# Performance work log

Measured on AMD Instinct MI355X. Metric: run time of the kernel, lower is better.

## Reference

```python
import jax, jax.numpy as jnp
import numpy as np

B, S, D, H, L = 128, 256, 128, 4, 2
N = S - 1            # tree nodes (complete binary tree, depths 0..7)
MAX_DEPTH = 7
NEG = -1e9
EPS = 1e-6


def _binary_tree_topology():
    n = np.arange(N)
    parent = np.where(n > 0, (n - 1) // 2, 0).astype(np.int32)   # parent(0) dummy
    depth = np.floor(np.log2(n + 1)).astype(np.int32)            # BFS level
    is_leaf = (2 * n + 1 >= N)
    return parent, depth, is_leaf


def setup_inputs() -> dict:
    key = jax.random.key(0)
    ks = jax.random.split(key, 6)
    p_np, d_np, l_np = _binary_tree_topology()
    parent = jnp.broadcast_to(jnp.asarray(p_np), (B, N))
    depth = jnp.broadcast_to(jnp.asarray(d_np), (B, N))
    is_leaf = jnp.broadcast_to(jnp.asarray(l_np), (B, N))
    x = jax.random.normal(ks[0], (B, S, D), jnp.float32)
    mask = jnp.zeros((B, 1, 1, S), jnp.float32)  # full trees -> no padding
    sc = 1.0 / np.sqrt(D)
    Wq = jax.random.normal(ks[1], (L, D, D), jnp.float32) * sc
    Wk = jax.random.normal(ks[2], (L, D, D), jnp.float32) * sc
    Wv = jax.random.normal(ks[3], (L, D, D), jnp.float32) * sc
    Wo = jax.random.normal(ks[4], (L, D, D), jnp.float32) * sc
    bq = jnp.zeros((L, D)); bk = jnp.zeros((L, D)); bv = jnp.zeros((L, D)); bo = jnp.zeros((L, D))
    g1 = jnp.ones((L, D)); b1 = jnp.zeros((L, D))
    g2 = jnp.ones((L, D)); b2 = jnp.zeros((L, D))
    return dict(x=x, mask=mask, parent=parent, depth=depth, is_leaf=is_leaf,
                Wq=Wq, bq=bq, Wk=Wk, bk=bk, Wv=Wv, bv=bv, Wo=Wo, bo=bo,
                g1=g1, b1=b1, g2=g2, b2=b2)


def _layernorm(x, g, b):
    mu = jnp.mean(x, axis=-1, keepdims=True)
    var = jnp.mean(jnp.square(x - mu), axis=-1, keepdims=True)
    return g * (x - mu) * jax.lax.rsqrt(var + EPS) + b


def _tree_agg(x, parent, depth, is_leaf):
    """Vectorized bottom-up tree aggregation (agg='sum': tanh(sum children)).
    Seq positions map to tree nodes in BFS order; last position passes through."""
    e = x[:, :N]                                            # [B, N, D]
    seg = (parent + (jnp.arange(B) * N)[:, None]).reshape(-1)  # flat parent ids
    for d in range(MAX_DEPTH, 0, -1):                       # deepest level -> root
        contrib = jnp.where((depth == d)[..., None], e, 0.0)
        agg = jax.ops.segment_sum(contrib.reshape(B * N, D), seg,
                                  num_segments=B * N).reshape(B, N, D)
        upd = ((depth == d - 1) & (~is_leaf))[..., None]    # internal nodes at d-1
        e = jnp.where(upd, jnp.tanh(agg), e)
    return jnp.concatenate([e, x[:, N:]], axis=1)


def reference(x, mask, parent, depth, is_leaf,
              Wq, bq, Wk, bk, Wv, bv, Wo, bo, g1, b1, g2, b2):
    Dh = D // H
    scale = 1.0 / jnp.sqrt(jnp.float32(Dh))
    losses = []
    weights = None
    for l in range(L):
        q = (jnp.einsum('bsd,de->bse', x, Wq[l]) + bq[l]).reshape(B, S, H, Dh).transpose(0, 2, 1, 3)
        k = (jnp.einsum('bsd,de->bse', x, Wk[l]) + bk[l]).reshape(B, S, H, Dh).transpose(0, 2, 1, 3)
        v = (jnp.einsum('bsd,de->bse', x, Wv[l]) + bv[l]).reshape(B, S, H, Dh).transpose(0, 2, 1, 3)
        logits = jnp.einsum('bhqd,bhkd->bhqk', q, k) * scale + mask * NEG
        attn = jax.nn.softmax(logits, axis=-1)              # [B, H, S, S]
        ctx = jnp.einsum('bhqk,bhkd->bhqd', attn, v).transpose(0, 2, 1, 3).reshape(B, S, D)
        att_out = jnp.einsum('bsd,de->bse', ctx, Wo[l]) + bo[l]
        out1 = _layernorm(x + att_out, g1[l], b1[l])
        tab = _tree_agg(out1, parent, depth, is_leaf)       # dropout: eval -> identity
        x = _layernorm(out1 + tab, g2[l], b2[l])
        weights = attn[:, :, -1, :]
        losses.append(jnp.sum(jnp.abs(weights)))
    total_l1 = jnp.sum(jnp.stack(losses))
    return x, total_l1, weights
```

## Files before the change

kernel.cpp:

```cpp
#include <hip/hip_runtime.h>
#include <math.h>

typedef __bf16 bf16x8 __attribute__((ext_vector_type(8)));
typedef __bf16 bf16x4 __attribute__((ext_vector_type(4)));
typedef __bf16 bf16x2 __attribute__((ext_vector_type(2)));
typedef float f32x4 __attribute__((ext_vector_type(4)));

namespace {
constexpr int kB = 128, kS = 256, kD = 128, kH = 4;
constexpr float kEps = 1e-6f;
constexpr float kScale = 0.17677669529663687f;
constexpr float kNeg = -1000000000.0f;
constexpr float kLog2e = 1.4426950408889634f;
constexpr size_t kSZ = (size_t)kB * kS * kD;
}

__device__ __forceinline__ void glds16(const void* g, void* l) {
    __builtin_amdgcn_global_load_lds(
        (const __attribute__((address_space(1))) unsigned int*)g,
        (__attribute__((address_space(3))) unsigned int*)l, 16, 0, 0);
}

__global__ __launch_bounds__(256) void wtrans(
    const float* __restrict__ Wq, const float* __restrict__ Wk,
    const float* __restrict__ Wv, const float* __restrict__ Wo,
    __bf16* __restrict__ Wt)
{
    const int mtx = blockIdx.x & 3, l = blockIdx.x >> 2;
    const float* W = (mtx == 0 ? Wq : mtx == 1 ? Wk : mtx == 2 ? Wv : Wo) +
                     (size_t)l * kD * kD;
    __bf16* o = Wt + (size_t)blockIdx.x * kD * kD;
    for (int idx = threadIdx.x; idx < kD * kD; idx += 256) {
        const int k = idx >> 7, n = idx & 127;
        const int lo = n & 15, ni = n >> 4;
        const int j = k & 7, tt = k >> 3, g = tt & 3, ks = tt >> 2;
        o[((ni * 4 + ks) * 64 + g * 16 + lo) * 8 + j] = (__bf16)W[idx];
    }
}

template <int WEIGHTS, bool F32X>
__global__ __launch_bounds__(512) void mega_attn(
    const void* __restrict__ xsrc, const __bf16* __restrict__ Wp,
    const float* __restrict__ bq, const float* __restrict__ bk,
    const float* __restrict__ bv, const float* __restrict__ bo,
    const float* __restrict__ mask, const float* __restrict__ gamma,
    const float* __restrict__ beta, __bf16* __restrict__ O1,
    float* __restrict__ wout, float* __restrict__ l1out)
{
    __shared__ __bf16 Xs[256 * 128];
    __shared__ __bf16 Kls[256 * 32];
    __shared__ __bf16 Vt[32][276];
    __shared__ __bf16 Pl[8][16 * 64];
    __shared__ __bf16 Qs[8][16 * 32];
    __shared__ __bf16 Ctx[128 * 128];
    __shared__ float mb[256];

    const int t = threadIdx.x;
    const int w = t >> 6, l = t & 63, lo = l & 15, g = l >> 4;
    const int b = blockIdx.x & 127, strip = blockIdx.x >> 7;
    const int q0 = strip * 128 + w * 16;
    const int tk0 = w * 32;
    const int kswz = (lo ^ (lo >> 2)) & 3;

    const __bf16* Wqp = Wp;
    const __bf16* Wkp = Wp + 16384;
    const __bf16* Wvp = Wp + 2 * 16384;
    const __bf16* Wop = Wp + 3 * 16384;

    if constexpr (F32X) {
#pragma unroll
        for (int p = 0; p < 8; ++p) {
            const int ci = p * 512 + t;
            const int row = ci >> 4, c = ci & 15;
            const float* src = (const float*)xsrc +
                               ((size_t)b * 256 + row) * 128 + c * 8;
            const float4 a0 = *(const float4*)src;
            const float4 a1 = *(const float4*)(src + 4);
            bf16x8 o;
            o[0] = (__bf16)a0.x; o[1] = (__bf16)a0.y; o[2] = (__bf16)a0.z; o[3] = (__bf16)a0.w;
            o[4] = (__bf16)a1.x; o[5] = (__bf16)a1.y; o[6] = (__bf16)a1.z; o[7] = (__bf16)a1.w;
            *(bf16x8*)&Xs[row * 128 + ((c ^ (row & 7)) << 3)] = o;
        }
    } else {
#pragma unroll
        for (int it = 0; it < 8; ++it)
            glds16((const __bf16*)xsrc + (size_t)b * 32768 + (it * 8 + w) * 512 + l * 8,
                   &Xs[(it * 8 + w) * 512]);
    }
    if (t < 256) mb[t] = mask[b * 256 + t] * (kNeg * kLog2e);
    if (WEIGHTS && blockIdx.x == 0 && t == 0) l1out[0] = 1024.0f;
    __syncthreads();

    auto wfrag = [&](const __bf16* W, int ni, int ks) {
        return *(const bf16x8*)(W + (((ni * 4 + ks) * 64 + l) << 3));
    };
    auto xfrag = [&](int row, int ks) {
        return *(const bf16x8*)&Xs[row * 128 + (((g + 4 * ks) ^ (row & 7)) << 3)];
    };

#pragma unroll
    for (int h = 0; h < 4; ++h) {
        bf16x8 xa[2][4];
#pragma unroll
        for (int mi = 0; mi < 2; ++mi)
#pragma unroll
            for (int ks = 0; ks < 4; ++ks)
                xa[mi][ks] = xfrag(tk0 + mi * 16 + lo, ks);

        f32x4 kacc[2][2], vacc[2][2];
#pragma unroll
        for (int i = 0; i < 2; ++i)
#pragma unroll
            for (int j2 = 0; j2 < 2; ++j2) {
                kacc[i][j2] = f32x4{0.f, 0.f, 0.f, 0.f};
                vacc[i][j2] = f32x4{0.f, 0.f, 0.f, 0.f};
            }
#pragma unroll
        for (int ks = 0; ks < 4; ++ks) {
            const bf16x8 wk0 = wfrag(Wkp, 2 * h, ks);
            const bf16x8 wk1 = wfrag(Wkp, 2 * h + 1, ks);
            const bf16x8 wv0 = wfrag(Wvp, 2 * h, ks);
            const bf16x8 wv1 = wfrag(Wvp, 2 * h + 1, ks);
            kacc[0][0] = __builtin_amdgcn_mfma_f32_16x16x32_bf16(wk0, xa[0][ks], kacc[0][0], 0, 0, 0);
            kacc[0][1] = __builtin_amdgcn_mfma_f32_16x16x32_bf16(wk0, xa[1][ks], kacc[0][1], 0, 0, 0);
            kacc[1][0] = __builtin_amdgcn_mfma_f32_16x16x32_bf16(wk1, xa[0][ks], kacc[1][0], 0, 0, 0);
            kacc[1][1] = __builtin_amdgcn_mfma_f32_16x16x32_bf16(wk1, xa[1][ks], kacc[1][1], 0, 0, 0);
            vacc[0][0] = __builtin_amdgcn_mfma_f32_16x16x32_bf16(xa[0][ks], wv0, vacc[0][0], 0, 0, 0);
            vacc[1][0] = __builtin_amdgcn_mfma_f32_16x16x32_bf16(xa[1][ks], wv0, vacc[1][0], 0, 0, 0);
            vacc[0][1] = __builtin_amdgcn_mfma_f32_16x16x32_bf16(xa[0][ks], wv1, vacc[0][1], 0, 0, 0);
            vacc[1][1] = __builtin_amdgcn_mfma_f32_16x16x32_bf16(xa[1][ks], wv1, vacc[1][1], 0, 0, 0);
        }
        f32x4 qacc[2] = {f32x4{0.f, 0.f, 0.f, 0.f}, f32x4{0.f, 0.f, 0.f, 0.f}};
#pragma unroll
        for (int ks = 0; ks < 4; ++ks) {
            const bf16x8 xq = xfrag(q0 + lo, ks);
            qacc[0] = __builtin_amdgcn_mfma_f32_16x16x32_bf16(xq, wfrag(Wqp, 2 * h, ks), qacc[0], 0, 0, 0);
            qacc[1] = __builtin_amdgcn_mfma_f32_16x16x32_bf16(xq, wfrag(Wqp, 2 * h + 1, ks), qacc[1], 0, 0, 0);
        }

#pragma unroll
        for (int dm = 0; dm < 2; ++dm) {
            const f32x4 bkv = *(const f32x4*)(bk + h * 32 + dm * 16 + 4 * g);
            const int pos = ((dm * 2 + (g >> 1)) ^ kswz) << 3;
            const int sub = (4 * g) & 7;
#pragma unroll
            for (int tj = 0; tj < 2; ++tj) {
                bf16x4 kv;
#pragma unroll
                for (int r = 0; r < 4; ++r) kv[r] = (__bf16)(kacc[dm][tj][r] + bkv[r]);
                const int key = tk0 + tj * 16 + lo;
                *(bf16x4*)&Kls[key * 32 + pos + sub] = kv;
            }
        }
#pragma unroll
        for (int nj = 0; nj < 2; ++nj) {
            const float bvv = bv[h * 32 + nj * 16 + lo];
#pragma unroll
            for (int mi = 0; mi < 2; ++mi) {
                bf16x4 vv4;
#pragma unroll
                for (int r = 0; r < 4; ++r) vv4[r] = (__bf16)(vacc[mi][nj][r] + bvv);
                *(bf16x4*)&Vt[nj * 16 + lo][tk0 + mi * 16 + 4 * g] = vv4;
            }
        }
#pragma unroll
        for (int nj = 0; nj < 2; ++nj) {
            const float bqv = bq[h * 32 + nj * 16 + lo];
#pragma unroll
            for (int r = 0; r < 4; ++r)
                Qs[w][(4 * g + r) * 32 + nj * 16 + lo] = (__bf16)(qacc[nj][r] + bqv);
        }
        __syncthreads();

        const bf16x8 qf = *(const bf16x8*)&Qs[w][lo * 32 + g * 8];
        f32x4 s[16];
        __builtin_amdgcn_s_setprio(1);
#pragma unroll
        for (int f = 0; f < 16; ++f) {
            const bf16x8 kf =
                *(const bf16x8*)&Kls[(f * 16 + lo) * 32 + ((g ^ kswz) << 3)];
            s[f] = __builtin_amdgcn_mfma_f32_16x16x32_bf16(
                kf, qf, f32x4{0.f, 0.f, 0.f, 0.f}, 0, 0, 0);
        }
        __builtin_amdgcn_s_setprio(0);

        float ls = 0.f;
#pragma unroll
        for (int f = 0; f < 16; ++f) {
            const f32x4 mk = *(const f32x4*)&mb[f * 16 + g * 4];
#pragma unroll
            for (int r = 0; r < 4; ++r) {
                const float p = __builtin_amdgcn_exp2f(
                    s[f][r] * (kScale * kLog2e) + mk[r]);
                s[f][r] = p;
                ls += p;
            }
        }
        ls += __shfl_xor(ls, 16, 64);
        ls += __shfl_xor(ls, 32, 64);

        if constexpr (WEIGHTS) {
            if (strip == 1 && w == 7 && lo == 15) {
                const float inv = 1.f / ls;
                float* wrow = wout + ((size_t)b * 4 + h) * 256;
#pragma unroll
                for (int f = 0; f < 16; ++f)
#pragma unroll
                    for (int r = 0; r < 4; ++r)
                        wrow[f * 16 + g * 4 + r] = s[f][r] * inv;
            }
        }

        f32x4 o[2] = {f32x4{0.f, 0.f, 0.f, 0.f}, f32x4{0.f, 0.f, 0.f, 0.f}};
#pragma unroll
        for (int qt = 0; qt < 4; ++qt) {
#pragma unroll
            for (int fl = 0; fl < 4; ++fl) {
                const int ff = qt * 4 + fl;
#pragma unroll
                for (int pr = 0; pr < 2; ++pr) {
                    bf16x2 pk;
                    pk[0] = (__bf16)s[ff][2 * pr];
                    pk[1] = (__bf16)s[ff][2 * pr + 1];
                    const int e = fl * 16 + 4 * g + 2 * pr;
                    const int addr =
                        lo * 64 + ((((e >> 3) ^ (lo & 7)) << 3) | (e & 7));
                    *(bf16x2*)&Pl[w][addr] = pk;
                }
            }
            __builtin_amdgcn_s_setprio(1);
#pragma unroll
            for (int ksl = 0; ksl < 2; ++ksl) {
                const int cc = ksl * 4 + g;
                const bf16x8 pa =
                    *(const bf16x8*)&Pl[w][lo * 64 + ((cc ^ (lo & 7)) << 3)];
#pragma unroll
                for (int nf = 0; nf < 2; ++nf) {
                    const bf16x8 bvv =
                        *(const bf16x8*)&Vt[nf * 16 + lo][(qt * 2 + ksl) * 32 + g * 8];
                    o[nf] = __builtin_amdgcn_mfma_f32_16x16x32_bf16(pa, bvv, o[nf], 0, 0, 0);
                }
            }
            __builtin_amdgcn_s_setprio(0);
        }

#pragma unroll
        for (int r = 0; r < 4; ++r) {
            const float inv = 1.f / __shfl(ls, 4 * g + r, 64);
            const int crow = w * 16 + g * 4 + r;
#pragma unroll
            for (int nf = 0; nf < 2; ++nf) {
                const int col = h * 32 + nf * 16 + lo;
                const int chunk = (col >> 3) ^ (crow & 7);
                Ctx[crow * 128 + (chunk << 3) + (col & 7)] = (__bf16)(o[nf][r] * inv);
            }
        }
        if (h < 3) __syncthreads();
    }

    const size_t m0 = (size_t)b * 256 + strip * 128;
    f32x4 acc[8];
#pragma unroll
    for (int ni = 0; ni < 8; ++ni) acc[ni] = f32x4{0.f, 0.f, 0.f, 0.f};

    const int arow = w * 16 + lo;
#pragma unroll
    for (int ks = 0; ks < 4; ++ks) {
        const bf16x8 av =
            *(const bf16x8*)&Ctx[arow * 128 + (((g + 4 * ks) ^ (arow & 7)) << 3)];
#pragma unroll
        for (int ni = 0; ni < 8; ++ni)
            acc[ni] = __builtin_amdgcn_mfma_f32_16x16x32_bf16(
                av, wfrag(Wop, ni, ks), acc[ni], 0, 0, 0);
    }

    float bcol[8], ga[8], be[8];
#pragma unroll
    for (int ni = 0; ni < 8; ++ni) {
        bcol[ni] = bo[ni * 16 + lo];
        ga[ni] = gamma[ni * 16 + lo];
        be[ni] = beta[ni * 16 + lo];
    }

    float vv[4][8];
    float s[4] = {0, 0, 0, 0}, s2[4] = {0, 0, 0, 0};
#pragma unroll
    for (int r = 0; r < 4; ++r) {
        const int local = strip * 128 + w * 16 + g * 4 + r;
#pragma unroll
        for (int ni = 0; ni < 8; ++ni) {
            const int col = ni * 16 + lo;
            const int chunk = (col >> 3) ^ (local & 7);
            const float rv = (float)Xs[local * 128 + (chunk << 3) + (col & 7)];
            const float x = acc[ni][r] + bcol[ni] + rv;
            vv[r][ni] = x; s[r] += x; s2[r] += x * x;
        }
    }
#pragma unroll
    for (int r = 0; r < 4; ++r)
#pragma unroll
        for (int o = 1; o < 16; o <<= 1) {
            s[r] += __shfl_xor(s[r], o, 64);
            s2[r] += __shfl_xor(s2[r], o, 64);
        }
#pragma unroll
    for (int r = 0; r < 4; ++r) {
        const float mu = s[r] * (1.f / 128.f);
        const float var = s2[r] * (1.f / 128.f) - mu * mu;
        const float rs = rsqrtf(var + kEps);
        const size_t mm = m0 + w * 16 + g * 4 + r;
#pragma unroll
        for (int ni = 0; ni < 8; ++ni)
            O1[mm * 128 + ni * 16 + lo] =
                (__bf16)(ga[ni] * (vv[r][ni] - mu) * rs + be[ni]);
    }
}

__global__ __launch_bounds__(1024) void tree_ln(
    const __bf16* __restrict__ o1, const float* __restrict__ gamma,
    const float* __restrict__ beta, float* __restrict__ xo,
    __bf16* __restrict__ xb, int wf32, int wbf16)
{
    __shared__ float e[127 * 132];
    const int isleaf = blockIdx.x >> 7;
    const int b = blockIdx.x & 127;
    const int t = threadIdx.x;
    const __bf16* ob = o1 + (size_t)b * 256 * 128;
    const int wv = t >> 6, lane = t & 63;
    const float2 gv = *(const float2*)(gamma + lane * 2);
    const float2 bb = *(const float2*)(beta + lane * 2);
    const int c = lane * 2;

    auto ln_store = [&](int row, float y0, float y1) {
        float s = y0 + y1, s2 = y0 * y0 + y1 * y1;
#pragma unroll
        for (int o = 1; o < 64; o <<= 1) {
            s += __shfl_xor(s, o, 64);
            s2 += __shfl_xor(s2, o, 64);
        }
        const float mu = s * (1.f / 128.f);
        const float var = s2 * (1.f / 128.f) - mu * mu;
        const float rs = rsqrtf(var + kEps);
        const float r0 = gv.x * (y0 - mu) * rs + bb.x;
        const float r1 = gv.y * (y1 - mu) * rs + bb.y;
        const size_t rowoff = ((size_t)b * 256 + row) * 128;
        if (wf32) {
            float2 o2; o2.x = r0; o2.y = r1;
            *(float2*)(xo + rowoff + c) = o2;
        }
        if (wbf16) {
            const int chunk = (c >> 3) ^ (row & 7);
            bf16x2 ob2; ob2[0] = (__bf16)r0; ob2[1] = (__bf16)r1;
            *(bf16x2*)(xb + rowoff + chunk * 8 + (c & 7)) = ob2;
        }
    };

    if (isleaf) {
        for (int row = 128 + wv; row < 256; row += 16) {
            const bf16x2 v = *(const bf16x2*)(ob + (size_t)row * 128 + c);
            ln_store(row, 2.f * (float)v[0], 2.f * (float)v[1]);
        }
        return;
    }

    {
        const int p = 63 + (t >> 4);
        const int cg = (t & 15) * 8;
        const bf16x8 c1 = *(const bf16x8*)(ob + (size_t)(2 * p + 1) * 128 + cg);
        const bf16x8 c2 = *(const bf16x8*)(ob + (size_t)(2 * p + 2) * 128 + cg);
        f32x4 r0, r1;
#pragma unroll
        for (int i = 0; i < 4; ++i)
            r0[i] = tanhf((float)c1[i] + (float)c2[i]);
#pragma unroll
        for (int i = 0; i < 4; ++i)
            r1[i] = tanhf((float)c1[4 + i] + (float)c2[4 + i]);
        *(f32x4*)&e[p * 132 + cg] = r0;
        *(f32x4*)&e[p * 132 + cg + 4] = r1;
    }
    __syncthreads();

    {
        const int col = wv * 8 + (lane & 7);
        const int nsub = lane >> 3;
        for (int lvl = 5; lvl >= 0; --lvl) {
            const int p0 = (1 << lvl) - 1;
            const int cnt = 1 << lvl;
            for (int base = 0; base < cnt; base += 8) {
                const int p = p0 + base + nsub;
                if (base + nsub < cnt) {
                    e[p * 132 + col] =
                        tanhf(e[(2 * p + 1) * 132 + col] + e[(2 * p + 2) * 132 + col]);
                }
            }
        }
    }
    __syncthreads();

    for (int row = wv; row < 128; row += 16) {
        const bf16x2 v = *(const bf16x2*)(ob + (size_t)row * 128 + c);
        float y0, y1;
        if (row < 127) {
            y0 = (float)v[0] + e[row * 132 + c];
            y1 = (float)v[1] + e[row * 132 + c + 1];
        } else {
            y0 = 2.f * (float)v[0];
            y1 = 2.f * (float)v[1];
        }
        ln_store(row, y0, y1);
    }
}

extern "C" void kernel_launch(void* const* d_in, const int* in_sizes, int n_in,
                              void* d_out, int out_size, void* d_ws, size_t ws_size,
                              hipStream_t stream)
{
    (void)in_sizes; (void)n_in; (void)out_size; (void)ws_size;

    const float* x_in = (const float*)d_in[0];
    const float* mask = (const float*)d_in[1];
    const float* Wq = (const float*)d_in[5];
    const float* bq = (const float*)d_in[6];
    const float* Wk = (const float*)d_in[7];
    const float* bk = (const float*)d_in[8];
    const float* Wv = (const float*)d_in[9];
    const float* bv = (const float*)d_in[10];
    const float* Wo = (const float*)d_in[11];
    const float* bo = (const float*)d_in[12];
    const float* g1 = (const float*)d_in[13];
    const float* b1 = (const float*)d_in[14];
    const float* g2 = (const float*)d_in[15];
    const float* b2 = (const float*)d_in[16];

    float* out_x = (float*)d_out;
    float* out_l1 = out_x + kSZ;
    float* out_w = out_l1 + 1;

    char* wsb = (char*)d_ws;
    __bf16* O1 = (__bf16*)wsb;
    __bf16* xb = (__bf16*)(wsb + kSZ * 2);
    __bf16* Wt = (__bf16*)(wsb + 2 * kSZ * 2);

    wtrans<<<8, 256, 0, stream>>>(Wq, Wk, Wv, Wo, Wt);

    mega_attn<0, true><<<256, 512, 0, stream>>>(x_in, Wt, bq, bk, bv, bo,
                                                mask, g1, b1, O1,
                                                nullptr, nullptr);
    tree_ln<<<256, 1024, 0, stream>>>(O1, g2, b2, nullptr, xb, 0, 1);

    mega_attn<1, false><<<256, 512, 0, stream>>>(xb, Wt + 4 * 16384,
                                                 bq + kD, bk + kD, bv + kD, bo + kD,
                                                 mask, g1 + kD, b1 + kD, O1,
                                                 out_w, out_l1);
    tree_ln<<<256, 1024, 0, stream>>>(O1, g2 + kD, b2 + kD, out_x, nullptr, 1, 0);
}
```

Measured before the change: 105.5 us.

## Software-pipeline next head's QKV projection MFMAs behind current head's attention

Hoists the X fragment loads (including the query rows) out of the per-head loop so they are read from LDS once. It also splits each head's K/V/Q projection into a compute phase and an LDS-write phase. The compute for head h+1 is issued right after head h's PV MFMAs, so the matrix work can overlap the softmax epilogue. The cost is an extra barrier per head and more live registers from the hoisted fragments and early accumulators, which may reduce occupancy or cause spills.

```diff
diff --git a/kernel.cpp b/kernel.cpp
--- a/kernel.cpp
+++ b/kernel.cpp
@@ -98,16 +98,17 @@
         return *(const bf16x8*)&Xs[row * 128 + (((g + 4 * ks) ^ (row & 7)) << 3)];
     };
 
-#pragma unroll
-    for (int h = 0; h < 4; ++h) {
-        bf16x8 xa[2][4];
-#pragma unroll
-        for (int mi = 0; mi < 2; ++mi)
-#pragma unroll
-            for (int ks = 0; ks < 4; ++ks)
-                xa[mi][ks] = xfrag(tk0 + mi * 16 + lo, ks);
-
-        f32x4 kacc[2][2], vacc[2][2];
+    bf16x8 xa[2][4], xq[4];
+#pragma unroll
+    for (int ks = 0; ks < 4; ++ks) {
+        xa[0][ks] = xfrag(tk0 + lo, ks);
+        xa[1][ks] = xfrag(tk0 + 16 + lo, ks);
+        xq[ks] = xfrag(q0 + lo, ks);
+    }
+
+    f32x4 kacc[2][2], vacc[2][2], qacc[2];
+
+    auto produce_compute = [&](int h) {
 #pragma unroll
         for (int i = 0; i < 2; ++i)
 #pragma unroll
@@ -115,6 +116,8 @@
                 kacc[i][j2] = f32x4{0.f, 0.f, 0.f, 0.f};
                 vacc[i][j2] = f32x4{0.f, 0.f, 0.f, 0.f};
             }
+        qacc[0] = f32x4{0.f, 0.f, 0.f, 0.f};
+        qacc[1] = f32x4{0.f, 0.f, 0.f, 0.f};
 #pragma unroll
         for (int ks = 0; ks < 4; ++ks) {
             const bf16x8 wk0 = wfrag(Wkp, 2 * h, ks);
@@ -129,15 +132,12 @@
             vacc[1][0] = __builtin_amdgcn_mfma_f32_16x16x32_bf16(xa[1][ks], wv0, vacc[1][0], 0, 0, 0);
             vacc[0][1] = __builtin_amdgcn_mfma_f32_16x16x32_bf16(xa[0][ks], wv1, vacc[0][1], 0, 0, 0);
             vacc[1][1] = __builtin_amdgcn_mfma_f32_16x16x32_bf16(xa[1][ks], wv1, vacc[1][1], 0, 0, 0);
-        }
-        f32x4 qacc[2] = {f32x4{0.f, 0.f, 0.f, 0.f}, f32x4{0.f, 0.f, 0.f, 0.f}};
-#pragma unroll
-        for (int ks = 0; ks < 4; ++ks) {
-            const bf16x8 xq = xfrag(q0 + lo, ks);
-            qacc[0] = __builtin_amdgcn_mfma_f32_16x16x32_bf16(xq, wfrag(Wqp, 2 * h, ks), qacc[0], 0, 0, 0);
-            qacc[1] = __builtin_amdgcn_mfma_f32_16x16x32_bf16(xq, wfrag(Wqp, 2 * h + 1, ks), qacc[1], 0, 0, 0);
-        }
-
+            qacc[0] = __builtin_amdgcn_mfma_f32_16x16x32_bf16(xq[ks], wfrag(Wqp, 2 * h, ks), qacc[0], 0, 0, 0);
+            qacc[1] = __builtin_amdgcn_mfma_f32_16x16x32_bf16(xq[ks], wfrag(Wqp, 2 * h + 1, ks), qacc[1], 0, 0, 0);
+        }
+    };
+
+    auto produce_write = [&](int h) {
 #pragma unroll
         for (int dm = 0; dm < 2; ++dm) {
             const f32x4 bkv = *(const f32x4*)(bk + h * 32 + dm * 16 + 4 * g);
@@ -170,8 +170,14 @@
             for (int r = 0; r < 4; ++r)
                 Qs[w][(4 * g + r) * 32 + nj * 16 + lo] = (__bf16)(qacc[nj][r] + bqv);
         }
-        __syncthreads();
-
+    };
+
+    produce_compute(0);
+    produce_write(0);
+    __syncthreads();
+
+#pragma unroll
+    for (int h = 0; h < 4; ++h) {
         const bf16x8 qf = *(const bf16x8*)&Qs[w][lo * 32 + g * 8];
         f32x4 s[16];
         __builtin_amdgcn_s_setprio(1);
@@ -244,6 +250,8 @@
             __builtin_amdgcn_s_setprio(0);
         }
 
+        if (h < 3) produce_compute(h + 1);
+
 #pragma unroll
         for (int r = 0; r < 4; ++r) {
             const float inv = 1.f / __shfl(ls, 4 * g + r, 64);
@@ -255,7 +263,11 @@
                 Ctx[crow * 128 + (chunk << 3) + (col & 7)] = (__bf16)(o[nf][r] * inv);
             }
         }
-        if (h < 3) __syncthreads();
+        if (h < 3) {
+            __syncthreads();
+            produce_write(h + 1);
+            __syncthreads();
+        }
     }
 
     const size_t m0 = (size_t)b * 256 + strip * 128;
```

After: 95.01 us. 1.11x faster.
